# Performance work log

Hardware: AMD Instinct MI355X
Metric: run time of the kernel (lower is better)

## Reference

```python
import jax, jax.numpy as jnp
import numpy as np

D = 1024
H = 16
DH = D // H
DFF = 4096
EPS = 1e-5


def new_gelu(u):
    # HF NewGELUActivation: 0.5*u*(1+tanh(sqrt(2/pi)*(u+0.044715*u^3)))
    c = np.sqrt(2.0 / np.pi).astype(np.float32)
    return 0.5 * u * (1.0 + jnp.tanh(c * (u + 0.044715 * u ** 3)))


def layer_norm(u, g, b):
    mu = jnp.mean(u, axis=-1, keepdims=True)
    var = jnp.mean((u - mu) ** 2, axis=-1, keepdims=True)
    return (u - mu) * jax.lax.rsqrt(var + EPS) * g + b


def setup_inputs() -> dict:
    key = jax.random.key(0)
    ks = jax.random.split(key, 12)
    s = 0.02
    inp = {
        "x": jax.random.normal(ks[0], (4, 1024, D), dtype=jnp.float32),
        "Wq": jax.random.normal(ks[1], (D, D), dtype=jnp.float32) * s,
        "bq": jnp.zeros((D,), jnp.float32),
        "Wk": jax.random.normal(ks[2], (D, D), dtype=jnp.float32) * s,
        "bk": jnp.zeros((D,), jnp.float32),
        "Wv": jax.random.normal(ks[3], (D, D), dtype=jnp.float32) * s,
        "bv": jnp.zeros((D,), jnp.float32),
        "Wo": jax.random.normal(ks[4], (D, D), dtype=jnp.float32) * s,
        "bo": jnp.zeros((D,), jnp.float32),
        "g1": jnp.ones((D,), jnp.float32),
        "b1": jnp.zeros((D,), jnp.float32),
        "W1": jax.random.normal(ks[5], (D, DFF), dtype=jnp.float32) * s,
        "bm1": jnp.zeros((DFF,), jnp.float32),
        "W2": jax.random.normal(ks[6], (DFF, D), dtype=jnp.float32) * s,
        "bm2": jnp.zeros((D,), jnp.float32),
        "g2": jnp.ones((D,), jnp.float32),
        "b2": jnp.zeros((D,), jnp.float32),
    }
    return inp


def reference(x, Wq, bq, Wk, bk, Wv, bv, Wo, bo, g1, b1, W1, bm1, W2, bm2, g2, b2):
    B, S, _ = x.shape
    q = (x @ Wq + bq).reshape(B, S, H, DH)
    k = (x @ Wk + bk).reshape(B, S, H, DH)
    v = (x @ Wv + bv).reshape(B, S, H, DH)
    scores = jnp.einsum("bshd,bthd->bhst", q, k) / np.sqrt(DH).astype(np.float32)
    probs = jax.nn.softmax(scores, axis=-1)
    attn = jnp.einsum("bhst,bthd->bshd", probs, v).reshape(B, S, D)
    attn = attn @ Wo + bo
    x1 = layer_norm(x + attn, g1, b1)
    mlp = new_gelu(x1 @ W1 + bm1) @ W2 + bm2
    out = layer_norm(x1 + mlp, g2, b2)
    return out
```

## Files before the change

kernel.cpp:

```cpp
#include <hip/hip_runtime.h>

#define D_    1024
#define HH    16
#define DHEAD 64
#define DFF_  4096
#define NTOK  4096
#define SQLEN 1024

typedef unsigned short ushort_t;
typedef __attribute__((ext_vector_type(8))) short short8;
typedef __attribute__((ext_vector_type(4))) float floatx4;

#define LOG2E 1.44269504f

__device__ __forceinline__ unsigned short f2bf(float f) {
  union { float f; unsigned u; } x; x.f = f;
  unsigned r = x.u + 0x7fffu + ((x.u >> 16) & 1u);
  return (unsigned short)(r >> 16);
}
__device__ __forceinline__ float bf2f(unsigned short u) {
  union { unsigned u; float f; } x; x.u = ((unsigned)u) << 16;
  return x.f;
}
__device__ __forceinline__ unsigned pack2bf_fast(float a, float b) {
  union { float f; unsigned u; } x, y; x.f = a; y.f = b;
  return __builtin_amdgcn_perm(y.u + 0x8000u, x.u + 0x8000u, 0x07060302u);
}
__device__ __forceinline__ float fast_exp2(float x) {
  return __builtin_amdgcn_exp2f(x);
}
__device__ __forceinline__ float fast_gelu(float u) {
  float u2 = u * u;
  float arg = u * (2.30220414f + 0.10294307f * u2);
  float e = __builtin_amdgcn_exp2f(arg);
  float r = __builtin_amdgcn_rcpf(e + 1.0f);
  return u - u * r;
}

__device__ __forceinline__ void async_ld16(const void* g, void* l) {
  __builtin_amdgcn_global_load_lds(
      (const __attribute__((address_space(1))) unsigned int*)g,
      (__attribute__((address_space(3))) unsigned int*)l, 16, 0, 0);
}

__device__ __forceinline__ unsigned lds_off(const void* p) {
  return (unsigned)(unsigned long long)
      (const __attribute__((address_space(3))) char*)p;
}
__device__ __forceinline__ short8 ds_read128(unsigned addr) {
  short8 r;
  asm volatile("ds_read_b128 %0, %1" : "=v"(r) : "v"(addr));
  return r;
}

__global__ __launch_bounds__(256) void prep_kernel(
    const float* __restrict__ x, const float* __restrict__ Wq,
    const float* __restrict__ Wk, const float* __restrict__ Wv,
    const float* __restrict__ Wo, const float* __restrict__ W1,
    const float* __restrict__ W2,
    ushort_t* __restrict__ xb, ushort_t* __restrict__ wqkvt,
    ushort_t* __restrict__ wot, ushort_t* __restrict__ w1t,
    ushort_t* __restrict__ w2t) {
  int bid = blockIdx.x, tid = threadIdx.x;
  if (bid < 4096) {
    int i = bid * 256 + tid;
    float4 v = ((const float4*)x)[i];
    ushort4 o;
    o.x = f2bf(v.x); o.y = f2bf(v.y); o.z = f2bf(v.z); o.w = f2bf(v.w);
    ((ushort4*)xb)[i] = o;
    return;
  }
  __shared__ float tile[32][33];
  const float* W; ushort_t* T; int K, N, n0, k0;
  if (bid < 8192) {
    int id = bid - 4096, z = id >> 10, xy = id & 1023;
    W = (z == 0) ? Wq : (z == 1) ? Wk : (z == 2) ? Wv : Wo;
    T = (z < 3) ? wqkvt + (size_t)z * D_ * D_ : wot;
    K = D_; N = D_;
    n0 = (xy & 31) * 32; k0 = (xy >> 5) * 32;
  } else if (bid < 12288) {
    int id = bid - 8192;
    W = W1; T = w1t; K = D_; N = DFF_;
    n0 = (id & 127) * 32; k0 = (id >> 7) * 32;
  } else {
    int id = bid - 12288;
    W = W2; T = w2t; K = DFF_; N = D_;
    n0 = (id & 31) * 32; k0 = (id >> 5) * 32;
  }
  int tx = tid & 31, ty = tid >> 5;
#pragma unroll
  for (int i = 0; i < 4; i++)
    tile[ty + i * 8][tx] = W[(size_t)(k0 + ty + i * 8) * N + n0 + tx];
  __syncthreads();
#pragma unroll
  for (int i = 0; i < 4; i++)
    T[(size_t)(n0 + ty + i * 8) * K + k0 + tx] = f2bf(tile[tx][ty + i * 8]);
}

template <int MODE>
__global__ __launch_bounds__(512, 2) void gemm256(
    const ushort_t* __restrict__ A, const ushort_t* __restrict__ Bt,
    int M, int N, int K, int Ks, int nb,
    const float* __restrict__ bias0, const float* __restrict__ bias1,
    const float* __restrict__ bias2,
    ushort_t* __restrict__ o0, ushort_t* __restrict__ o1, ushort_t* __restrict__ o2) {
  __shared__ alignas(16) ushort_t sA[2][2][128 * 64];
  __shared__ alignas(16) ushort_t sB[2][2][128 * 64];
  int tid = threadIdx.x;
  int w = tid >> 6, lane = tid & 63, quad = lane >> 4, l16 = lane & 15;
  int wm = w >> 2, wn = w & 3;

  int sp = blockIdx.x / nb;
  int bid = blockIdx.x - sp * nb;
  int gridN = N >> 8;
  int Tn = nb >> 3;
  int lin = (bid & 7) * Tn + (bid >> 3);
  int ng = gridN << 3;
  int gidx = lin / ng;
  int rem = lin - gidx * ng;
  int m0 = ((gidx << 3) + (rem & 7)) << 8;
  int n0 = (rem >> 3) << 8;
  int kbeg = sp * Ks;
  int nkt = Ks >> 6;

  floatx4 acc[8][4];
#pragma unroll
  for (int i = 0; i < 8; i++)
#pragma unroll
    for (int j = 0; j < 4; j++) acc[i][j] = (floatx4){0.f, 0.f, 0.f, 0.f};

  int s8  = tid >> 3;
  int lcx = (tid & 7) ^ (s8 & 7);
  const ushort_t* gA = A + (size_t)(m0 + s8) * K + kbeg + lcx * 8;
  const ushort_t* gB = Bt + (size_t)(n0 + (s8 & 31) + (s8 >> 5) * 64) * K + kbeg + lcx * 8;
  char* sta = (char*)&sA[0][0][0] + w * 1024;
  char* stb = (char*)&sB[0][0][0] + w * 1024;

  unsigned kof0 = (unsigned)((quad ^ (l16 & 7)) << 4);
  unsigned baseA = lds_off(&sA[0][0][0]) + (unsigned)((wm * 64 + l16) * 128);
  unsigned baseB = lds_off(&sB[0][0][0]) + (unsigned)((wn * 32 + l16) * 128);

#define STG_A(db, h, ko) { const ushort_t* _g = gA + (size_t)(h) * 64 * K + (ko); \
    char* _l = sta + (db) * 32768 + (h) * 16384; \
    async_ld16(_g, _l); async_ld16(_g + (size_t)128 * K, _l + 8192); }
#define STG_B(db, h, ko) { const ushort_t* _g = gB + (size_t)(h) * 32 * K + (ko); \
    char* _l = stb + (db) * 32768 + (h) * 16384; \
    async_ld16(_g, _l); async_ld16(_g + (size_t)128 * K, _l + 8192); }
#define LD_A(db, mq) { unsigned _p = baseA + (db) * 32768u + (mq) * 16384u + kof0; \
    _Pragma("unroll") for (int mt = 0; mt < 4; mt++) { \
      a[mt][0] = ds_read128(_p + (unsigned)(mt * 2048)); \
      a[mt][1] = ds_read128((_p + (unsigned)(mt * 2048)) ^ 64u); } }
#define LD_B(db, nq) { unsigned _p = baseB + (db) * 32768u + (nq) * 16384u + kof0; \
    _Pragma("unroll") for (int nt = 0; nt < 2; nt++) { \
      b[nt][0] = ds_read128(_p + (unsigned)(nt * 2048)); \
      b[nt][1] = ds_read128((_p + (unsigned)(nt * 2048)) ^ 64u); } }
#define MFMA_Q(mq, nq) { \
    _Pragma("unroll") for (int mt = 0; mt < 4; mt++) \
    _Pragma("unroll") for (int nt = 0; nt < 2; nt++) { \
      floatx4 c = acc[(mq) * 4 + mt][(nq) * 2 + nt]; \
      c = __builtin_amdgcn_mfma_f32_16x16x32_bf16(a[mt][0], b[nt][0], c, 0, 0, 0); \
      c = __builtin_amdgcn_mfma_f32_16x16x32_bf16(a[mt][1], b[nt][1], c, 0, 0, 0); \
      acc[(mq) * 4 + mt][(nq) * 2 + nt] = c; } }
#define BAR __builtin_amdgcn_s_barrier()
#define LGK0 { asm volatile("s_waitcnt lgkmcnt(0)" ::: "memory"); \
               __builtin_amdgcn_sched_barrier(0); }
#define VMW4 asm volatile("s_waitcnt vmcnt(4)" ::: "memory")
#define VMW2 asm volatile("s_waitcnt vmcnt(2)" ::: "memory")
#define VMW0 asm volatile("s_waitcnt vmcnt(0)" ::: "memory")
#define PRIO1 __builtin_amdgcn_s_setprio(1)
#define PRIO0 __builtin_amdgcn_s_setprio(0)

  short8 a[4][2], b[2][2];

  STG_A(0, 0, 0); STG_B(0, 0, 0); STG_B(0, 1, 0); STG_A(0, 1, 0);
  VMW4; BAR;

  for (int kt = 0; kt + 1 < nkt; kt++) {
    int db = kt & 1, dn = db ^ 1;
    int ko = (kt + 1) << 6;
    LD_A(db, 0); LD_B(db, 0);
    STG_A(dn, 0, ko);
    BAR; LGK0;
    PRIO1; MFMA_Q(0, 0); PRIO0;
    VMW4; BAR;
    LD_B(db, 1);
    STG_B(dn, 0, ko);
    BAR; LGK0;
    PRIO1; MFMA_Q(0, 1); PRIO0;
    VMW4; BAR;
    LD_A(db, 1);
    STG_B(dn, 1, ko);
    BAR; LGK0;
    PRIO1; MFMA_Q(1, 1); PRIO0;
    BAR;
    LD_B(db, 0);
    STG_A(dn, 1, ko);
    BAR; LGK0;
    PRIO1; MFMA_Q(1, 0); PRIO0;
    VMW4; BAR;
  }
  {
    int db = (nkt - 1) & 1;
    LD_A(db, 0); LD_B(db, 0);
    BAR; LGK0;
    PRIO1; MFMA_Q(0, 0); PRIO0;
    VMW2; BAR;
    LD_B(db, 1);
    BAR; LGK0;
    PRIO1; MFMA_Q(0, 1); PRIO0;
    VMW0; BAR;
    LD_A(db, 1);
    BAR; LGK0;
    PRIO1; MFMA_Q(1, 1); PRIO0;
    BAR;
    LD_B(db, 0);
    BAR; LGK0;
    PRIO1; MFMA_Q(1, 0); PRIO0;
  }

  if (MODE == 0) {
#pragma unroll
    for (int bj = 0; bj < 4; bj++) {
      int cg = n0 + wn * 64 + (bj >> 1) * 32 + (bj & 1) * 16 + l16;
      int sel = cg >> 10, nn = cg & 1023;
      const float* bpp = (sel == 0) ? bias0 : ((sel == 1) ? bias1 : bias2);
      float bb = bpp[nn];
      int hh = nn >> 6, dd = nn & 63;
#pragma unroll
      for (int ai = 0; ai < 8; ai++) {
        int rg0 = m0 + wm * 128 + (ai >> 2) * 64 + (ai & 3) * 16 + quad * 4;
        int b0 = rg0 >> 10, s0 = rg0 & 1023;
        if (sel == 2) {
          ushort4 ov;
          ov.x = f2bf(acc[ai][bj][0] + bb);
          ov.y = f2bf(acc[ai][bj][1] + bb);
          ov.z = f2bf(acc[ai][bj][2] + bb);
          ov.w = f2bf(acc[ai][bj][3] + bb);
          *(ushort4*)(o2 + ((size_t)(b0 * HH + hh) * DHEAD + dd) * SQLEN + s0) = ov;
        } else {
          ushort_t* dst = sel ? o1 : o0;
          float sc = (sel == 0) ? (0.125f * LOG2E) : 1.0f;
#pragma unroll
          for (int r = 0; r < 4; r++)
            dst[((size_t)(b0 * HH + hh) * SQLEN + s0 + r) * DHEAD + dd] =
                f2bf((acc[ai][bj][r] + bb) * sc);
        }
      }
    }
  } else {
    size_t rowbase = (size_t)(m0 + wm * 128 + quad * 4) * N + (n0 + wn * 64 + l16);
    if (MODE == 3) rowbase += (size_t)sp * M * N;
    float bb[4];
    if (MODE == 2) {
#pragma unroll
      for (int c = 0; c < 4; c++)
        bb[c] = bias0[(n0 + wn * 64 + c * 16 + l16) & (N - 1)];
    }
#pragma unroll
    for (int ai = 0; ai < 8; ai++) {
#pragma unroll
      for (int r = 0; r < 4; r++) {
        ushort_t* pr = o0 + rowbase + (size_t)((ai >> 2) * 64 + (ai & 3) * 16 + r) * N;
        if (MODE == 2) {
          pr[0]  = f2bf(fast_gelu(acc[ai][0][r] + bb[0]));
          pr[16] = f2bf(fast_gelu(acc[ai][1][r] + bb[1]));
          pr[32] = f2bf(fast_gelu(acc[ai][2][r] + bb[2]));
          pr[48] = f2bf(fast_gelu(acc[ai][3][r] + bb[3]));
        } else {
          pr[0]  = f2bf(acc[ai][0][r]);
          pr[16] = f2bf(acc[ai][1][r]);
          pr[32] = f2bf(acc[ai][2][r]);
          pr[48] = f2bf(acc[ai][3][r]);
        }
      }
    }
  }
#undef STG_A
#undef STG_B
#undef LD_A
#undef LD_B
#undef MFMA_Q
#undef BAR
#undef LGK0
#undef VMW4
#undef VMW2
#undef VMW0
#undef PRIO1
#undef PRIO0
}

__global__ __launch_bounds__(256) void flash_attn_kernel(const ushort_t* __restrict__ q,
                                                         const ushort_t* __restrict__ k,
                                                         const ushort_t* __restrict__ vt,
                                                         ushort_t* __restrict__ ctx) {
  __shared__ alignas(16) ushort_t sQ[2][128 * 32];
  __shared__ alignas(16) ushort_t sK[2][64 * 32];
  __shared__ alignas(16) ushort_t sVt[2][64 * 32];
  __shared__ alignas(16) char sP[4][2][2][16 * 80];
  int tid = threadIdx.x;
  int w = tid >> 6, lane = tid & 63, quad = lane >> 4, l16 = lane & 15;
  int bh = blockIdx.x, qt = blockIdx.y;
  int b_ = bh >> 4, h_ = bh & 15;

  const ushort_t* Qp = q + ((size_t)bh * SQLEN + qt * 128) * DHEAD;
  const ushort_t* Kp = k + (size_t)bh * SQLEN * DHEAD;
  const ushort_t* Vtp = vt + (size_t)bh * DHEAD * SQLEN;

  int srow = lane >> 2, scol8 = (lane & 3) * 8;

#pragma unroll
  for (int h = 0; h < 2; h++)
#pragma unroll
    for (int p = 0; p < 2; p++)
      async_ld16(Qp + (h * 64 + w * 16 + srow) * 64 + p * 32 + scol8,
                 (char*)sQ + p * 8192 + (h * 64 + w * 16) * 64);

  float l_run[2] = {0.f, 0.f};
  floatx4 o_acc[2][4];
#pragma unroll
  for (int g = 0; g < 2; g++)
#pragma unroll
    for (int dt = 0; dt < 4; dt++) o_acc[g][dt] = (floatx4){0.f, 0.f, 0.f, 0.f};

  for (int kt = 0; kt < 16; kt++) {
    __syncthreads();
#pragma unroll
    for (int t = 0; t < 2; t++) {
      int id = w * 2 + t, panel = id & 1, rg = id >> 1;
      int row = rg * 16 + srow, col = panel * 32 + scol8;
      async_ld16(Kp + kt * 64 * 64 + row * 64 + col,
                 (char*)sK + panel * 4096 + rg * 1024);
      async_ld16(Vtp + (size_t)row * SQLEN + kt * 64 + col,
                 (char*)sVt + panel * 4096 + rg * 1024);
    }
    __syncthreads();

    floatx4 st[2][4];
#pragma unroll
    for (int g = 0; g < 2; g++)
#pragma unroll
      for (int nt = 0; nt < 4; nt++) st[g][nt] = (floatx4){0.f, 0.f, 0.f, 0.f};
#pragma unroll
    for (int kc = 0; kc < 2; kc++) {
      short8 aq0 = *(const short8*)(sQ[kc] + (w * 32 + l16) * 32 + quad * 8);
      short8 aq1 = *(const short8*)(sQ[kc] + (w * 32 + 16 + l16) * 32 + quad * 8);
#pragma unroll
      for (int nt = 0; nt < 4; nt++) {
        short8 kf = *(const short8*)(sK[kc] + (nt * 16 + l16) * 32 + quad * 8);
        st[0][nt] = __builtin_amdgcn_mfma_f32_16x16x32_bf16(kf, aq0, st[0][nt], 0, 0, 0);
        st[1][nt] = __builtin_amdgcn_mfma_f32_16x16x32_bf16(kf, aq1, st[1][nt], 0, 0, 0);
      }
    }

#pragma unroll
    for (int g = 0; g < 2; g++) {
#pragma unroll
      for (int nt = 0; nt < 4; nt++) {
        float p0 = fast_exp2(st[g][nt][0]);
        float p1 = fast_exp2(st[g][nt][1]);
        float p2 = fast_exp2(st[g][nt][2]);
        float p3 = fast_exp2(st[g][nt][3]);
        l_run[g] += (p0 + p1) + (p2 + p3);
        uint2 d2;
        d2.x = pack2bf_fast(p0, p1);
        d2.y = pack2bf_fast(p2, p3);
        *(uint2*)(&sP[w][g][nt >> 1][0] + l16 * 80 + (nt & 1) * 32 + quad * 8) = d2;
      }
    }

#pragma unroll
    for (int kc = 0; kc < 2; kc++) {
      short8 pf0 = *(const short8*)(&sP[w][0][kc][0] + l16 * 80 + quad * 16);
      short8 pf1 = *(const short8*)(&sP[w][1][kc][0] + l16 * 80 + quad * 16);
#pragma unroll
      for (int dt = 0; dt < 4; dt++) {
        short8 vf = *(const short8*)(sVt[kc] + (dt * 16 + l16) * 32 + quad * 8);
        o_acc[0][dt] = __builtin_amdgcn_mfma_f32_16x16x32_bf16(vf, pf0, o_acc[0][dt], 0, 0, 0);
        o_acc[1][dt] = __builtin_amdgcn_mfma_f32_16x16x32_bf16(vf, pf1, o_acc[1][dt], 0, 0, 0);
      }
    }
  }

#pragma unroll
  for (int g = 0; g < 2; g++) {
    float l = l_run[g];
    l += __shfl_xor(l, 16);
    l += __shfl_xor(l, 32);
    float inv = 1.f / fmaxf(l, 1e-30f);
    int s_ = qt * 128 + w * 32 + g * 16 + l16;
    ushort_t* cp = ctx + (size_t)(b_ * SQLEN + s_) * D_ + h_ * DHEAD + quad * 4;
#pragma unroll
    for (int dt = 0; dt < 4; dt++) {
      ushort4 ov;
      ov.x = f2bf(o_acc[g][dt][0] * inv);
      ov.y = f2bf(o_acc[g][dt][1] * inv);
      ov.z = f2bf(o_acc[g][dt][2] * inv);
      ov.w = f2bf(o_acc[g][dt][3] * inv);
      *(ushort4*)(cp + dt * 16) = ov;
    }
  }
}

template <int S, int WB>
__global__ __launch_bounds__(256) void ln_red_kernel(
    const ushort_t* __restrict__ parts, const float* __restrict__ bias,
    const float* __restrict__ res, const float* __restrict__ g,
    const float* __restrict__ b, float* __restrict__ outf,
    ushort_t* __restrict__ outb) {
  int row = blockIdx.x, tid = threadIdx.x;
  float4 v = ((const float4*)(res + (size_t)row * D_))[tid];
  float4 bb = ((const float4*)bias)[tid];
  v.x += bb.x; v.y += bb.y; v.z += bb.z; v.w += bb.w;
#pragma unroll
  for (int s = 0; s < S; s++) {
    ushort4 p = ((const ushort4*)(parts + (size_t)s * NTOK * D_ + (size_t)row * D_))[tid];
    v.x += bf2f(p.x); v.y += bf2f(p.y); v.z += bf2f(p.z); v.w += bf2f(p.w);
  }
  float s1 = v.x + v.y + v.z + v.w;
  float s2 = v.x * v.x + v.y * v.y + v.z * v.z + v.w * v.w;
#pragma unroll
  for (int off = 32; off > 0; off >>= 1) {
    s1 += __shfl_down(s1, off);
    s2 += __shfl_down(s2, off);
  }
  __shared__ float red[10];
  int wid = tid >> 6, lane = tid & 63;
  if (lane == 0) { red[wid] = s1; red[4 + wid] = s2; }
  __syncthreads();
  if (tid == 0) {
    float ts = red[0] + red[1] + red[2] + red[3];
    float ts2 = red[4] + red[5] + red[6] + red[7];
    float mu = ts * (1.f / 1024.f);
    float var = ts2 * (1.f / 1024.f) - mu * mu;
    red[8] = mu;
    red[9] = rsqrtf(var + 1e-5f);
  }
  __syncthreads();
  float mu = red[8], rsg = red[9];
  float4 gv = ((const float4*)g)[tid];
  float4 bv = ((const float4*)b)[tid];
  float4 o;
  o.x = (v.x - mu) * rsg * gv.x + bv.x;
  o.y = (v.y - mu) * rsg * gv.y + bv.y;
  o.z = (v.z - mu) * rsg * gv.z + bv.z;
  o.w = (v.w - mu) * rsg * gv.w + bv.w;
  if (outf) ((float4*)(outf + (size_t)row * D_))[tid] = o;
  if (WB) {
    ushort4 ob;
    ob.x = f2bf(o.x); ob.y = f2bf(o.y); ob.z = f2bf(o.z); ob.w = f2bf(o.w);
    ((ushort4*)(outb + (size_t)row * D_))[tid] = ob;
  }
}

extern "C" void kernel_launch(void* const* d_in, const int* in_sizes, int n_in,
                              void* d_out, int out_size, void* d_ws, size_t ws_size,
                              hipStream_t stream) {
  const float* x   = (const float*)d_in[0];
  const float* Wq  = (const float*)d_in[1];
  const float* bq  = (const float*)d_in[2];
  const float* Wk  = (const float*)d_in[3];
  const float* bk  = (const float*)d_in[4];
  const float* Wv  = (const float*)d_in[5];
  const float* bv  = (const float*)d_in[6];
  const float* Wo  = (const float*)d_in[7];
  const float* bo  = (const float*)d_in[8];
  const float* g1  = (const float*)d_in[9];
  const float* b1  = (const float*)d_in[10];
  const float* W1  = (const float*)d_in[11];
  const float* bm1 = (const float*)d_in[12];
  const float* W2  = (const float*)d_in[13];
  const float* bm2 = (const float*)d_in[14];
  const float* g2  = (const float*)d_in[15];
  const float* b2  = (const float*)d_in[16];
  float* out = (float*)d_out;

  char* ws = (char*)d_ws;
  const size_t MB = 1024 * 1024;
  ushort_t* xb    = (ushort_t*)(ws + 0);
  ushort_t* wqkvt = (ushort_t*)(ws + 8 * MB);
  ushort_t* wot   = (ushort_t*)(ws + 14 * MB);
  ushort_t* w1t   = (ushort_t*)(ws + 16 * MB);
  ushort_t* w2t   = (ushort_t*)(ws + 24 * MB);
  ushort_t* qb    = (ushort_t*)(ws + 32 * MB);
  ushort_t* kb    = (ushort_t*)(ws + 40 * MB);
  ushort_t* vtb   = (ushort_t*)(ws + 48 * MB);
  ushort_t* ctx   = (ushort_t*)(ws + 56 * MB);
  float*    x1    = (float*)   (ws + 64 * MB);
  ushort_t* x1b   = (ushort_t*)(ws + 80 * MB);
  ushort_t* hbuf  = (ushort_t*)(ws + 88 * MB);
  ushort_t* pWo   = (ushort_t*)(ws + 88 * MB);
  ushort_t* pMd   = (ushort_t*)(ws + 32 * MB);
  (void)ws_size; (void)in_sizes; (void)n_in; (void)out_size;

  hipLaunchKernelGGL(prep_kernel, dim3(16384), dim3(256), 0, stream,
                     x, Wq, Wk, Wv, Wo, W1, W2, xb, wqkvt, wot, w1t, w2t);

  hipLaunchKernelGGL((gemm256<0>), dim3(192), dim3(512), 0, stream,
                     xb, wqkvt, NTOK, 3072, D_, 1024, 192, bq, bk, bv, qb, kb, vtb);

  hipLaunchKernelGGL(flash_attn_kernel, dim3(4 * HH, SQLEN / 128), dim3(256), 0, stream,
                     qb, kb, vtb, ctx);

  hipLaunchKernelGGL((gemm256<3>), dim3(256), dim3(512), 0, stream,
                     ctx, wot, NTOK, D_, D_, 256, 64,
                     (const float*)nullptr, (const float*)nullptr,
                     (const float*)nullptr, pWo, (ushort_t*)nullptr, (ushort_t*)nullptr);

  hipLaunchKernelGGL((ln_red_kernel<4, 1>), dim3(NTOK), dim3(256), 0, stream,
                     pWo, bo, x, g1, b1, x1, x1b);

  hipLaunchKernelGGL((gemm256<2>), dim3(256), dim3(512), 0, stream,
                     x1b, w1t, NTOK, DFF_, D_, 1024, 256, bm1, (const float*)nullptr,
                     (const float*)nullptr, hbuf, (ushort_t*)nullptr, (ushort_t*)nullptr);

  hipLaunchKernelGGL((gemm256<3>), dim3(256), dim3(512), 0, stream,
                     hbuf, w2t, NTOK, D_, DFF_, 1024, 64,
                     (const float*)nullptr, (const float*)nullptr,
                     (const float*)nullptr, pMd, (ushort_t*)nullptr, (ushort_t*)nullptr);

  hipLaunchKernelGGL((ln_red_kernel<4, 0>), dim3(NTOK), dim3(256), 0, stream,
                     pMd, bm2, x1, g2, b2, out, (ushort_t*)nullptr);
}
```

Measured before the change: 318.9 us.

## Software-pipeline LDS fragment reads ahead of MFMAs with extra register buffers

Restructures the GEMM main loop so LDS fragment reads for the next quadrant are issued before the current quadrant's MFMAs, using separate register buffers and partial lgkmcnt waits. The loop is unrolled by two k-tiles to alternate buffers. Launch bounds drop to one block per SIMD pair, freeing registers for the extra fragments but reducing occupancy. The fixed pairing assumes an even tile count, and the barrier placement needs care to avoid LDS races.

```diff
diff --git a/kernel.cpp b/kernel.cpp
--- a/kernel.cpp
+++ b/kernel.cpp
@@ -98,7 +98,7 @@
 }
 
 template <int MODE>
-__global__ __launch_bounds__(512, 2) void gemm256(
+__global__ __launch_bounds__(512, 1) void gemm256(
     const ushort_t* __restrict__ A, const ushort_t* __restrict__ Bt,
     int M, int N, int K, int Ks, int nb,
     const float* __restrict__ bias0, const float* __restrict__ bias1,
@@ -146,76 +146,72 @@
 #define STG_B(db, h, ko) { const ushort_t* _g = gB + (size_t)(h) * 32 * K + (ko); \
     char* _l = stb + (db) * 32768 + (h) * 16384; \
     async_ld16(_g, _l); async_ld16(_g + (size_t)128 * K, _l + 8192); }
-#define LD_A(db, mq) { unsigned _p = baseA + (db) * 32768u + (mq) * 16384u + kof0; \
+#define LDSA(db, mq, DST) { unsigned _p = baseA + (db) * 32768u + (mq) * 16384u + kof0; \
     _Pragma("unroll") for (int mt = 0; mt < 4; mt++) { \
-      a[mt][0] = ds_read128(_p + (unsigned)(mt * 2048)); \
-      a[mt][1] = ds_read128((_p + (unsigned)(mt * 2048)) ^ 64u); } }
-#define LD_B(db, nq) { unsigned _p = baseB + (db) * 32768u + (nq) * 16384u + kof0; \
+      DST[mt][0] = ds_read128(_p + (unsigned)(mt * 2048)); \
+      DST[mt][1] = ds_read128((_p + (unsigned)(mt * 2048)) ^ 64u); } }
+#define LDSB(db, nq, DST) { unsigned _p = baseB + (db) * 32768u + (nq) * 16384u + kof0; \
     _Pragma("unroll") for (int nt = 0; nt < 2; nt++) { \
-      b[nt][0] = ds_read128(_p + (unsigned)(nt * 2048)); \
-      b[nt][1] = ds_read128((_p + (unsigned)(nt * 2048)) ^ 64u); } }
-#define MFMA_Q(mq, nq) { \
+      DST[nt][0] = ds_read128(_p + (unsigned)(nt * 2048)); \
+      DST[nt][1] = ds_read128((_p + (unsigned)(nt * 2048)) ^ 64u); } }
+#define MFMAC(mq, nq, A_, B_) { \
     _Pragma("unroll") for (int mt = 0; mt < 4; mt++) \
     _Pragma("unroll") for (int nt = 0; nt < 2; nt++) { \
       floatx4 c = acc[(mq) * 4 + mt][(nq) * 2 + nt]; \
-      c = __builtin_amdgcn_mfma_f32_16x16x32_bf16(a[mt][0], b[nt][0], c, 0, 0, 0); \
-      c = __builtin_amdgcn_mfma_f32_16x16x32_bf16(a[mt][1], b[nt][1], c, 0, 0, 0); \
+      c = __builtin_amdgcn_mfma_f32_16x16x32_bf16(A_[mt][0], B_[nt][0], c, 0, 0, 0); \
+      c = __builtin_amdgcn_mfma_f32_16x16x32_bf16(A_[mt][1], B_[nt][1], c, 0, 0, 0); \
       acc[(mq) * 4 + mt][(nq) * 2 + nt] = c; } }
 #define BAR __builtin_amdgcn_s_barrier()
-#define LGK0 { asm volatile("s_waitcnt lgkmcnt(0)" ::: "memory"); \
-               __builtin_amdgcn_sched_barrier(0); }
+#define LGKC(n) { asm volatile("s_waitcnt lgkmcnt(" #n ")" ::: "memory"); \
+                  __builtin_amdgcn_sched_barrier(0); }
 #define VMW4 asm volatile("s_waitcnt vmcnt(4)" ::: "memory")
 #define VMW2 asm volatile("s_waitcnt vmcnt(2)" ::: "memory")
 #define VMW0 asm volatile("s_waitcnt vmcnt(0)" ::: "memory")
 #define PRIO1 __builtin_amdgcn_s_setprio(1)
 #define PRIO0 __builtin_amdgcn_s_setprio(0)
 
-  short8 a[4][2], b[2][2];
+  short8 aP[4][2], aQ[4][2], b0A[2][2], b0B[2][2], b1[2][2];
 
   STG_A(0, 0, 0); STG_B(0, 0, 0); STG_B(0, 1, 0); STG_A(0, 1, 0);
   VMW4; BAR;
-
-  for (int kt = 0; kt + 1 < nkt; kt++) {
-    int db = kt & 1, dn = db ^ 1;
-    int ko = (kt + 1) << 6;
-    LD_A(db, 0); LD_B(db, 0);
-    STG_A(dn, 0, ko);
-    BAR; LGK0;
-    PRIO1; MFMA_Q(0, 0); PRIO0;
-    VMW4; BAR;
-    LD_B(db, 1);
-    STG_B(dn, 0, ko);
-    BAR; LGK0;
-    PRIO1; MFMA_Q(0, 1); PRIO0;
-    VMW4; BAR;
-    LD_A(db, 1);
-    STG_B(dn, 1, ko);
-    BAR; LGK0;
-    PRIO1; MFMA_Q(1, 1); PRIO0;
-    BAR;
-    LD_B(db, 0);
-    STG_A(dn, 1, ko);
-    BAR; LGK0;
-    PRIO1; MFMA_Q(1, 0); PRIO0;
-    VMW4; BAR;
+  LDSA(0, 0, aP); LDSB(0, 0, b0A);
+  VMW2; BAR;
+
+  for (int kt = 0; kt + 2 < nkt; kt += 2) {
+    int ko1 = (kt + 1) << 6, ko2 = (kt + 2) << 6;
+    LDSB(0, 1, b1);                 STG_A(1, 0, ko1);
+    LGKC(4);  PRIO1; MFMAC(0, 0, aP, b0A); PRIO0; VMW2; BAR;
+    LDSA(0, 1, aQ);                 STG_B(1, 0, ko1);
+    LGKC(8);  PRIO1; MFMAC(0, 1, aP, b1);  PRIO0;       BAR;
+                                    STG_B(1, 1, ko1);
+    LGKC(0);  PRIO1; MFMAC(1, 1, aQ, b1);  PRIO0; VMW2; BAR;
+    LDSA(1, 0, aP); LDSB(1, 0, b0B); STG_A(1, 1, ko1);
+              PRIO1; MFMAC(1, 0, aQ, b0A); PRIO0; VMW2; BAR;
+    LDSB(1, 1, b1);                 STG_A(0, 0, ko2);
+    LGKC(4);  PRIO1; MFMAC(0, 0, aP, b0B); PRIO0; VMW2; BAR;
+    LDSA(1, 1, aQ);                 STG_B(0, 0, ko2);
+    LGKC(8);  PRIO1; MFMAC(0, 1, aP, b1);  PRIO0;       BAR;
+                                    STG_B(0, 1, ko2);
+    LGKC(0);  PRIO1; MFMAC(1, 1, aQ, b1);  PRIO0; VMW2; BAR;
+    LDSA(0, 0, aP); LDSB(0, 0, b0A); STG_A(0, 1, ko2);
+              PRIO1; MFMAC(1, 0, aQ, b0B); PRIO0; VMW2; BAR;
   }
   {
-    int db = (nkt - 1) & 1;
-    LD_A(db, 0); LD_B(db, 0);
-    BAR; LGK0;
-    PRIO1; MFMA_Q(0, 0); PRIO0;
-    VMW2; BAR;
-    LD_B(db, 1);
-    BAR; LGK0;
-    PRIO1; MFMA_Q(0, 1); PRIO0;
-    VMW0; BAR;
-    LD_A(db, 1);
-    BAR; LGK0;
-    PRIO1; MFMA_Q(1, 1); PRIO0;
-    BAR;
-    LD_B(db, 0);
-    BAR; LGK0;
-    PRIO1; MFMA_Q(1, 0); PRIO0;
+    int ko1 = (nkt - 1) << 6;
+    LDSB(0, 1, b1);                 STG_A(1, 0, ko1);
+    LGKC(4);  PRIO1; MFMAC(0, 0, aP, b0A); PRIO0; VMW2; BAR;
+    LDSA(0, 1, aQ);                 STG_B(1, 0, ko1);
+    LGKC(8);  PRIO1; MFMAC(0, 1, aP, b1);  PRIO0;       BAR;
+                                    STG_B(1, 1, ko1);
+    LGKC(0);  PRIO1; MFMAC(1, 1, aQ, b1);  PRIO0; VMW2; BAR;
+    LDSA(1, 0, aP); LDSB(1, 0, b0B); STG_A(1, 1, ko1);
+              PRIO1; MFMAC(1, 0, aQ, b0A); PRIO0; VMW2; BAR;
+    LDSB(1, 1, b1);
+    LGKC(4);  PRIO1; MFMAC(0, 0, aP, b0B); PRIO0; VMW0; BAR;
+    LDSA(1, 1, aQ);
+    LGKC(8);  PRIO1; MFMAC(0, 1, aP, b1);  PRIO0;
+    LGKC(0);  PRIO1; MFMAC(1, 1, aQ, b1);  PRIO0;
+              PRIO1; MFMAC(1, 0, aQ, b0B); PRIO0;
   }
 
   if (MODE == 0) {
@@ -277,11 +273,11 @@
   }
 #undef STG_A
 #undef STG_B
-#undef LD_A
-#undef LD_B
-#undef MFMA_Q
+#undef LDSA
+#undef LDSB
+#undef MFMAC
 #undef BAR
-#undef LGK0
+#undef LGKC
 #undef VMW4
 #undef VMW2
 #undef VMW0
```

After: 620.0 us. +94.4%, slower.
